# Optimization experiments

Hardware: AMD Instinct MI355X
Metric: run time of the kernel (lower is better)

Reference implementation:

```python
import jax, jax.numpy as jnp
import numpy as np

B, S = 32, 128
E_NUM, SKILL, D_K, D_E, D_A = 4000, 256, 128, 128, 128
AT_NUM, IT_NUM = 1000, 1000
GAMMA = 0.03


def _lin(key, out_d, in_d):
    # xavier-normal style init
    w = jax.random.normal(key, (out_d, in_d), jnp.float32) * (2.0 / (in_d + out_d)) ** 0.5
    b = jnp.zeros((out_d,), jnp.float32)
    return w, b


def setup_inputs() -> dict:
    key = jax.random.key(0)
    ks = jax.random.split(key, 16)
    exercise_id = jax.random.randint(ks[0], (B, S), 0, E_NUM, jnp.int32)
    ans_time = jax.random.randint(ks[1], (B, S), 0, AT_NUM, jnp.int32)
    interval_time = jax.random.randint(ks[2], (B, S), 0, IT_NUM, jnp.int32)
    answer_value = jax.random.randint(ks[3], (B, S), 0, 2, jnp.int32)
    # enhanced q-matrix: binary with zeros replaced by gamma
    qmask = jax.random.bernoulli(ks[4], 0.1, (E_NUM, SKILL))
    q_matrix = jnp.where(qmask, 1.0, GAMMA).astype(jnp.float32)
    ex_table = jax.random.normal(ks[5], (E_NUM, D_E), jnp.float32)
    at_table = jax.random.normal(ks[6], (AT_NUM, D_K), jnp.float32)
    it_table = jax.random.normal(ks[7], (IT_NUM, D_K), jnp.float32)
    W1, b1 = _lin(ks[8], D_K, D_E + D_K + D_A)   # learning_embed_layer
    Wl, bl = _lin(ks[9], D_K, 4 * D_K)           # learning_layer
    Wg, bg = _lin(ks[10], D_K, 4 * D_K)          # learning_gate
    Wf, bf = _lin(ks[11], D_K, 3 * D_K)          # forgetting_gate
    Wp, bp = _lin(ks[12], D_K, 2 * D_K)          # predicting_layer
    # xavier-uniform initial knowledge state, shared across batch
    lim = (6.0 / (SKILL + D_K)) ** 0.5
    h0 = jax.random.uniform(ks[13], (SKILL, D_K), jnp.float32, -lim, lim)
    return {"exercise_id": exercise_id, "ans_time": ans_time,
            "interval_time": interval_time, "answer_value": answer_value,
            "q_matrix": q_matrix, "ex_table": ex_table, "at_table": at_table,
            "it_table": it_table, "W1": W1, "b1": b1, "Wl": Wl, "bl": bl,
            "Wg": Wg, "bg": bg, "Wf": Wf, "bf": bf, "Wp": Wp, "bp": bp, "h0": h0}


def _forward(exercise_id, ans_time, interval_time, answer_value, q_matrix,
             ex_table, at_table, it_table, W1, b1, Wl, bl, Wg, bg, Wf, bf,
             Wp, bp, h0):
    b, s = exercise_id.shape
    ex = ex_table[exercise_id]                       # (B,S,d_e)
    at = at_table[ans_time]                          # (B,S,d_k)
    it = it_table[interval_time]                     # (B,S,d_k)
    ans = jnp.broadcast_to(answer_value.astype(ex.dtype)[..., None], (b, s, D_A))
    le = jnp.concatenate([ex, at, ans], -1) @ W1.T + b1   # learning embedding (B,S,d_k)
    kv = q_matrix[exercise_id]                       # knowledge vectors (B,S,skill)

    h_pre = jnp.broadcast_to(h0, (b,) + h0.shape)    # (B,skill,d_k)
    h_tilde_pre = jnp.einsum('bs,bsd->bd', kv[:, 0], h_pre)
    learning_pre = jnp.zeros((b, D_K), ex.dtype)

    def step(carry, xs):
        h_pre, h_tilde_pre, learning_pre = carry
        lv, itv, kv_t, kv_next, ex_next = xs
        x4 = jnp.concatenate([learning_pre, itv, lv, h_tilde_pre], -1)
        lg = jnp.tanh(x4 @ Wl.T + bl)
        gate = jax.nn.sigmoid(x4 @ Wg.T + bg)
        LG = gate * (lg + 1.0) * 0.5                 # (B,d_k)
        LG_tilde = kv_t[:, :, None] * LG[:, None, :] # outer product addressing (B,skill,d_k)
        x3 = jnp.concatenate([h_pre,
                              jnp.broadcast_to(LG[:, None, :], h_pre.shape),
                              jnp.broadcast_to(itv[:, None, :], h_pre.shape)], -1)
        f = jax.nn.sigmoid(x3 @ Wf.T + bf)           # forget gate per skill
        h = LG_tilde + f * h_pre                     # updated knowledge state
        h_tilde = jnp.einsum('bs,bsd->bd', kv_next, h)
        pred = jax.nn.sigmoid(jnp.concatenate([ex_next, h_tilde], -1) @ Wp.T + bp)
        return (h, h_tilde, lv), pred

    sw = lambda a: jnp.swapaxes(a, 0, 1)
    xs = (sw(le[:, :-1]), sw(it[:, 1:]), sw(kv[:, :-1]), sw(kv[:, 1:]), sw(ex[:, 1:]))
    _, preds = jax.lax.scan(step, (h_pre, h_tilde_pre, learning_pre), xs)
    return jnp.swapaxes(preds, 0, 1)                 # (B, S-1, d_k)


def reference(exercise_id, ans_time, interval_time, answer_value, q_matrix,
              ex_table, at_table, it_table, W1, b1, Wl, bl, Wg, bg, Wf, bf,
              Wp, bp, h0):
    return _forward(exercise_id, ans_time, interval_time, answer_value, q_matrix,
                    ex_table, at_table, it_table, W1, b1, Wl, bl, Wg, bg, Wf, bf,
                    Wp, bp, h0)
```

## Files before the change

kernel.cpp:

```cpp
#include <hip/hip_runtime.h>

typedef unsigned int u32;
typedef unsigned short u16;
typedef unsigned long long u64;
typedef u16 u16x8 __attribute__((ext_vector_type(8)));
typedef u16 u16x4 __attribute__((ext_vector_type(4)));
typedef __bf16 bf16x8 __attribute__((ext_vector_type(8)));
typedef __bf16 bf16x4v __attribute__((ext_vector_type(4)));
typedef float f32x4 __attribute__((ext_vector_type(4)));
typedef float f32x2 __attribute__((ext_vector_type(2)));

#define B_SZ 32
#define S_SZ 128
#define T_SZ 127
#define DK 128
#define SKILL 256
#define SQTR 64
#define RL 136
#define PP 68
#define NPAIR 8
#define SPIN_CAP (1 << 18)

__device__ __forceinline__ u16x4 cvt4(f32x4 v) {
    return __builtin_bit_cast(u16x4, __builtin_convertvector(v, bf16x4v));
}
__device__ __forceinline__ u16x8 cvt8(f32x4 a, f32x4 b) {
    u16x4 x = cvt4(a), y = cvt4(b);
    u16x8 r;
    r[0]=x[0]; r[1]=x[1]; r[2]=x[2]; r[3]=x[3];
    r[4]=y[0]; r[5]=y[1]; r[6]=y[2]; r[7]=y[3];
    return r;
}
__device__ __forceinline__ u16 bfu(float x) {
    return __builtin_bit_cast(u16, (__bf16)x);
}
__device__ __forceinline__ float sigm(float x) {
    float e = __builtin_amdgcn_exp2f(-1.44269504f * x);
    return __builtin_amdgcn_rcpf(1.f + e);
}
__device__ __forceinline__ float tanh_f(float x) {
    float e = __builtin_amdgcn_exp2f(-2.88539008f * x);
    return 2.f * __builtin_amdgcn_rcpf(1.f + e) - 1.f;
}
__device__ __forceinline__ f32x4 mfma16(u16x8 a, u16x8 bb, f32x4 c) {
    return __builtin_amdgcn_mfma_f32_16x16x32_bf16(
        __builtin_bit_cast(bf16x8, a), __builtin_bit_cast(bf16x8, bb), c, 0, 0, 0);
}
__device__ __forceinline__ float pval(u64 p) {
    return __builtin_bit_cast(float, (u32)p);
}
__device__ __forceinline__ float dot4(f32x4 w, f32x4 x) {
    return w[0] * x[0] + w[1] * x[1] + w[2] * x[2] + w[3] * x[3];
}

__global__ __launch_bounds__(128, 2) void k_le(
    const int* __restrict__ eid, const int* __restrict__ atime,
    const int* __restrict__ ansv, const float* __restrict__ ex_t,
    const float* __restrict__ at_t, const float* __restrict__ W1,
    const float* __restrict__ b1, float* __restrict__ le_ws)
{
    const int o = threadIdx.x;
    const int p0 = blockIdx.x * NPAIR;
    int eP[NPAIR], aP[NPAIR];
    float avP[NPAIR];
    #pragma unroll
    for (int i = 0; i < NPAIR; ++i) {
        int p = p0 + i, b = p / T_SZ, t = p - b * T_SZ;
        int idx = b * S_SZ + t;
        eP[i] = eid[idx];
        aP[i] = atime[idx];
        avP[i] = (float)ansv[idx];
    }
    const float* wr = W1 + o * 384;
    const float bias = b1[o];
    float acc[NPAIR];
    #pragma unroll
    for (int i = 0; i < NPAIR; ++i) acc[i] = bias;
    #pragma unroll 2
    for (int k4 = 0; k4 < 32; ++k4) {
        f32x4 w = *(const f32x4*)(wr + 4 * k4);
        #pragma unroll
        for (int i = 0; i < NPAIR; ++i) {
            f32x4 x = *(const f32x4*)(ex_t + eP[i] * DK + 4 * k4);
            acc[i] += dot4(w, x);
        }
    }
    #pragma unroll 2
    for (int k4 = 32; k4 < 64; ++k4) {
        f32x4 w = *(const f32x4*)(wr + 4 * k4);
        #pragma unroll
        for (int i = 0; i < NPAIR; ++i) {
            f32x4 x = *(const f32x4*)(at_t + aP[i] * DK + 4 * k4 - 128);
            acc[i] += dot4(w, x);
        }
    }
    float wsum = 0.f;
    #pragma unroll 4
    for (int k4 = 64; k4 < 96; ++k4) {
        f32x4 w = *(const f32x4*)(wr + 4 * k4);
        wsum += w[0] + w[1] + w[2] + w[3];
    }
    #pragma unroll
    for (int i = 0; i < NPAIR; ++i)
        le_ws[(p0 + i) * DK + o] = acc[i] + avP[i] * wsum;
}

__global__ __launch_bounds__(128, 2) void k_pre(
    const int* __restrict__ itime, const float* __restrict__ it_t,
    const float* __restrict__ Wl, const float* __restrict__ blv,
    const float* __restrict__ Wg, const float* __restrict__ bgv,
    const float* __restrict__ Wf, const float* __restrict__ bfv,
    const float* __restrict__ le_ws,
    float* __restrict__ PRE_l, float* __restrict__ PRE_g, float* __restrict__ PRE_f)
{
    const int o = threadIdx.x;
    const int p0 = blockIdx.x * NPAIR;
    int ivP[NPAIR], lpOff[NPAIR];
    float mP[NPAIR];
    #pragma unroll
    for (int i = 0; i < NPAIR; ++i) {
        int p = p0 + i, b = p / T_SZ, t = p - b * T_SZ;
        ivP[i] = itime[b * S_SZ + t + 1];
        mP[i] = (t == 0) ? 0.f : 1.f;
        lpOff[i] = ((t == 0) ? p : p - 1) * DK;
    }
    const float* wl = Wl + o * 512;
    const float* wg = Wg + o * 512;
    const float bl0 = blv[o], bg0 = bgv[o];
    float al[NPAIR], ag[NPAIR];
    #pragma unroll
    for (int i = 0; i < NPAIR; ++i) { al[i] = bl0; ag[i] = bg0; }
    #pragma unroll 2
    for (int k4 = 0; k4 < 32; ++k4) {
        f32x4 w  = *(const f32x4*)(wl + 4 * k4);
        f32x4 w2 = *(const f32x4*)(wg + 4 * k4);
        #pragma unroll
        for (int i = 0; i < NPAIR; ++i) {
            f32x4 x = *(const f32x4*)(le_ws + lpOff[i] + 4 * k4);
            #pragma unroll
            for (int j = 0; j < 4; ++j) {
                float xv = x[j] * mP[i];
                al[i] += w[j] * xv;
                ag[i] += w2[j] * xv;
            }
        }
    }
    #pragma unroll 2
    for (int k4 = 0; k4 < 32; ++k4) {
        f32x4 w  = *(const f32x4*)(wl + 128 + 4 * k4);
        f32x4 w2 = *(const f32x4*)(wg + 128 + 4 * k4);
        #pragma unroll
        for (int i = 0; i < NPAIR; ++i) {
            f32x4 x = *(const f32x4*)(it_t + ivP[i] * DK + 4 * k4);
            #pragma unroll
            for (int j = 0; j < 4; ++j) {
                al[i] += w[j] * x[j];
                ag[i] += w2[j] * x[j];
            }
        }
    }
    #pragma unroll 2
    for (int k4 = 0; k4 < 32; ++k4) {
        f32x4 w  = *(const f32x4*)(wl + 256 + 4 * k4);
        f32x4 w2 = *(const f32x4*)(wg + 256 + 4 * k4);
        #pragma unroll
        for (int i = 0; i < NPAIR; ++i) {
            f32x4 x = *(const f32x4*)(le_ws + (p0 + i) * DK + 4 * k4);
            #pragma unroll
            for (int j = 0; j < 4; ++j) {
                al[i] += w[j] * x[j];
                ag[i] += w2[j] * x[j];
            }
        }
    }
    const float bf0 = bfv[o];
    float af[NPAIR];
    #pragma unroll
    for (int i = 0; i < NPAIR; ++i) af[i] = bf0;
    const float* wf = Wf + o * 384 + 256;
    #pragma unroll 2
    for (int k4 = 0; k4 < 32; ++k4) {
        f32x4 w = *(const f32x4*)(wf + 4 * k4);
        #pragma unroll
        for (int i = 0; i < NPAIR; ++i) {
            f32x4 x = *(const f32x4*)(it_t + ivP[i] * DK + 4 * k4);
            af[i] += dot4(w, x);
        }
    }
    #pragma unroll
    for (int i = 0; i < NPAIR; ++i) {
        size_t idx = (size_t)(p0 + i) * DK + o;
        PRE_l[idx] = al[i];
        PRE_g[idx] = ag[i];
        PRE_f[idx] = af[i];
    }
}

__global__ __launch_bounds__(512, 1) void k_main(
    const int* __restrict__ eid, const float* __restrict__ qmat,
    const float* __restrict__ Wl, const float* __restrict__ Wg,
    const float* __restrict__ Wf, const float* __restrict__ h0,
    const float* __restrict__ PRE_l, const float* __restrict__ PRE_g,
    const float* __restrict__ PRE_f, float* __restrict__ ht_ws,
    u64* __restrict__ xbuf)
{
    extern __shared__ char smem[];
    u16*   hS   = (u16*)smem;
    float* part = (float*)(smem + 17408);
    u16*   htbf = (u16*)(smem + 52224);
    u16*   LGb  = (u16*)(smem + 52736);
    float* LGf  = (float*)(smem + 53248);
    float* cS   = (float*)(smem + 53760);

    const int b    = blockIdx.x;
    const int qid  = blockIdx.y;
    const int tid  = threadIdx.x;
    const int w    = tid >> 6;
    const int lane = tid & 63;
    const int quad = lane >> 4;
    const int l4   = lane & 15;
    const int ih   = w & 1;
    const int jh   = w >> 1;

    u64* xq = xbuf + (size_t)b * 1024;
    const int qa = (qid + 1) & 3, qb2 = (qid + 2) & 3, qc = (qid + 3) & 3;

    u16x8 afr[4][4];
    #pragma unroll
    for (int mt = 0; mt < 4; ++mt)
        #pragma unroll
        for (int kt = 0; kt < 4; ++kt) {
            const float* p = Wf + (64 * ih + 16 * mt + l4) * 384 + 32 * kt + quad * 8;
            afr[mt][kt] = cvt8(*(const f32x4*)p, *(const f32x4*)(p + 4));
        }
    u16x8 azf[2][4];
    #pragma unroll
    for (int mt = 0; mt < 2; ++mt)
        #pragma unroll
        for (int kt = 0; kt < 4; ++kt) {
            int d = 16 * w + 8 * mt + (l4 >> 1);
            const float* base = (l4 & 1) ? Wg : Wl;
            const float* p = base + d * 512 + 384 + 32 * kt + quad * 8;
            azf[mt][kt] = cvt8(*(const f32x4*)p, *(const f32x4*)(p + 4));
        }
    u16x8 acf[4];
    #pragma unroll
    for (int kt = 0; kt < 4; ++kt) {
        const float* p = Wf + (16 * w + l4) * 384 + 128 + 32 * kt + quad * 8;
        acf[kt] = cvt8(*(const f32x4*)p, *(const f32x4*)(p + 4));
    }

    const int sl = 16 * jh + l4;
    f32x4 hreg[4];
    #pragma unroll
    for (int mt = 0; mt < 4; ++mt) {
        int d0 = 64 * ih + 16 * mt + quad * 4;
        f32x4 hv = *(const f32x4*)(h0 + (SQTR * qid + sl) * DK + d0);
        hreg[mt] = hv;
        *(u16x4*)(hS + sl * RL + d0) = cvt4(hv);
    }

    float kvt = qmat[eid[b * S_SZ] * SKILL + SQTR * qid + sl];

    f32x4 accF[4];

    {
        float htp[16];
        #pragma unroll
        for (int mt = 0; mt < 4; ++mt)
            #pragma unroll
            for (int r = 0; r < 4; ++r)
                htp[mt * 4 + r] = kvt * hreg[mt][r];
        #pragma unroll
        for (int mt = 0; mt < 4; ++mt)
            #pragma unroll
            for (int r = 0; r < 4; ++r)
                part[(64 * ih + 16 * mt + quad * 4 + r) * PP + jh * 16 + l4] = htp[mt * 4 + r];
        __syncthreads();
        int d = tid >> 2, kq = tid & 3;
        const float* pp = part + d * PP + kq * 16;
        float v = 0.f;
        #pragma unroll
        for (int i4 = 0; i4 < 4; ++i4) {
            f32x4 x = *(const f32x4*)(pp + 4 * i4);
            v += x[0] + x[1] + x[2] + x[3];
        }
        v += __shfl_xor(v, 1, 64);
        v += __shfl_xor(v, 2, 64);
        if (kq == 0) {
            u64 pkt = ((u64)1u << 32) | (u64)__builtin_bit_cast(u32, v);
            __hip_atomic_store(xq + qid * 256 + 128 + d, pkt,
                               __ATOMIC_RELAXED, __HIP_MEMORY_SCOPE_AGENT);
        }
        asm volatile("" ::: "memory");
        #pragma unroll
        for (int mt = 0; mt < 4; ++mt)
            accF[mt] = (f32x4){0.f, 0.f, 0.f, 0.f};
        {
            const u16* bp2 = hS + sl * RL + quad * 8;
            u16x8 bfr[4];
            #pragma unroll
            for (int kt = 0; kt < 4; ++kt) bfr[kt] = *(const u16x8*)(bp2 + kt * 32);
            #pragma unroll
            for (int mt = 0; mt < 4; ++mt)
                #pragma unroll
                for (int kt = 0; kt < 4; ++kt)
                    accF[mt] = mfma16(afr[mt][kt], bfr[kt], accF[mt]);
        }
        if (kq == 0) {
            u64 pa, pb, pc2;
            int spins = 0;
            do {
                pa  = __hip_atomic_load(xq + qa * 256 + 128 + d, __ATOMIC_RELAXED, __HIP_MEMORY_SCOPE_AGENT);
                pb  = __hip_atomic_load(xq + qb2 * 256 + 128 + d, __ATOMIC_RELAXED, __HIP_MEMORY_SCOPE_AGENT);
                pc2 = __hip_atomic_load(xq + qc * 256 + 128 + d, __ATOMIC_RELAXED, __HIP_MEMORY_SCOPE_AGENT);
                if ((u32)(pa >> 32) >= 1u && (u32)(pb >> 32) >= 1u && (u32)(pc2 >> 32) >= 1u) break;
                if (spins > 64) __builtin_amdgcn_s_sleep(1);
            } while (++spins < SPIN_CAP);
            float va = pval(pa), vb = pval(pb), vc = pval(pc2);
            float v0 = (qid == 0) ? v : (qid == 3) ? va : (qid == 2) ? vb : vc;
            float v1 = (qid == 1) ? v : (qid == 0) ? va : (qid == 3) ? vb : vc;
            float v2 = (qid == 2) ? v : (qid == 1) ? va : (qid == 0) ? vb : vc;
            float v3 = (qid == 3) ? v : (qid == 2) ? va : (qid == 1) ? vb : vc;
            float vt = ((v0 + v1) + v2) + v3;
            float hf = (float)(__bf16)vt;
            htbf[d] = bfu(vt);
            htbf[128 + d] = bfu(vt - hf);
        }
        __syncthreads();
    }

    for (int t = 0; t < T_SZ; ++t) {
        const size_t tb = (size_t)(b * T_SZ + t) * DK;
        float kvn = qmat[eid[b * S_SZ + t + 1] * SKILL + SQTR * qid + sl];
        f32x2 pl[2], pg[2];
        #pragma unroll
        for (int mt = 0; mt < 2; ++mt) {
            int d0 = 16 * w + 8 * mt + 2 * quad;
            pl[mt] = *(const f32x2*)(PRE_l + tb + d0);
            pg[mt] = *(const f32x2*)(PRE_g + tb + d0);
        }
        f32x4 pf = *(const f32x4*)(PRE_f + tb + 16 * w + quad * 4);

        f32x4 accZ[2];
        accZ[0] = (f32x4){0.f, 0.f, 0.f, 0.f};
        accZ[1] = (f32x4){0.f, 0.f, 0.f, 0.f};
        #pragma unroll
        for (int kt = 0; kt < 4; ++kt) {
            u16x8 bh = *(const u16x8*)(htbf + 32 * kt + quad * 8);
            u16x8 bl = *(const u16x8*)(htbf + 128 + 32 * kt + quad * 8);
            #pragma unroll
            for (int mt = 0; mt < 2; ++mt) {
                accZ[mt] = mfma16(azf[mt][kt], bh, accZ[mt]);
                accZ[mt] = mfma16(azf[mt][kt], bl, accZ[mt]);
            }
        }
        #pragma unroll
        for (int mt = 0; mt < 2; ++mt) {
            u32 hpack = 0, lpack = 0;
            f32x2 fpack;
            #pragma unroll
            for (int rp = 0; rp < 2; ++rp) {
                float zl = accZ[mt][2 * rp] + pl[mt][rp];
                float zg = accZ[mt][2 * rp + 1] + pg[mt][rp];
                float LGv = sigm(zg) * (tanh_f(zl) + 1.f) * 0.5f;
                float hif = (float)(__bf16)LGv;
                hpack |= ((u32)bfu(LGv)) << (16 * rp);
                lpack |= ((u32)bfu(LGv - hif)) << (16 * rp);
                fpack[rp] = LGv;
            }
            if (l4 == 0) {
                int d0 = 16 * w + 8 * mt + 2 * quad;
                *(u32*)(LGb + d0) = hpack;
                *(u32*)(LGb + 128 + d0) = lpack;
                *(f32x2*)(LGf + d0) = fpack;
            }
        }
        __syncthreads();

        {
            f32x4 accC = (f32x4){0.f, 0.f, 0.f, 0.f};
            #pragma unroll
            for (int kt = 0; kt < 4; ++kt) {
                u16x8 bh = *(const u16x8*)(LGb + 32 * kt + quad * 8);
                u16x8 bl = *(const u16x8*)(LGb + 128 + 32 * kt + quad * 8);
                accC = mfma16(acf[kt], bh, accC);
                accC = mfma16(acf[kt], bl, accC);
            }
            accC += pf;
            if (l4 == 0) *(f32x4*)(cS + 16 * w + quad * 4) = accC;
        }
        __syncthreads();

        float htp[16];
        #pragma unroll
        for (int mt = 0; mt < 4; ++mt) {
            int d0 = 64 * ih + 16 * mt + quad * 4;
            f32x4 lg = *(const f32x4*)(LGf + d0);
            f32x4 cc = *(const f32x4*)(cS + d0);
            f32x4 hv;
            #pragma unroll
            for (int r = 0; r < 4; ++r) {
                float f = sigm(accF[mt][r] + cc[r]);
                float hn = kvt * lg[r] + f * hreg[mt][r];
                hreg[mt][r] = hn;
                htp[mt * 4 + r] = kvn * hn;
                hv[r] = hn;
            }
            *(u16x4*)(hS + sl * RL + d0) = cvt4(hv);
        }
        #pragma unroll
        for (int mt = 0; mt < 4; ++mt)
            #pragma unroll
            for (int r = 0; r < 4; ++r)
                part[(64 * ih + 16 * mt + quad * 4 + r) * PP + jh * 16 + l4] = htp[mt * 4 + r];
        kvt = kvn;
        __syncthreads();

        {
            int d = tid >> 2, kq = tid & 3;
            const float* pp = part + d * PP + kq * 16;
            float v = 0.f;
            #pragma unroll
            for (int i4 = 0; i4 < 4; ++i4) {
                f32x4 x = *(const f32x4*)(pp + 4 * i4);
                v += x[0] + x[1] + x[2] + x[3];
            }
            v += __shfl_xor(v, 1, 64);
            v += __shfl_xor(v, 2, 64);
            const int slot = t & 1;
            const u32 seq = (u32)(t + 2);
            if (kq == 0) {
                u64 pkt = ((u64)seq << 32) | (u64)__builtin_bit_cast(u32, v);
                __hip_atomic_store(xq + qid * 256 + slot * 128 + d, pkt,
                                   __ATOMIC_RELAXED, __HIP_MEMORY_SCOPE_AGENT);
            }
            asm volatile("" ::: "memory");
            #pragma unroll
            for (int mt = 0; mt < 4; ++mt)
                accF[mt] = (f32x4){0.f, 0.f, 0.f, 0.f};
            {
                const u16* bp2 = hS + sl * RL + quad * 8;
                u16x8 bfr[4];
                #pragma unroll
                for (int kt = 0; kt < 4; ++kt) bfr[kt] = *(const u16x8*)(bp2 + kt * 32);
                #pragma unroll
                for (int mt = 0; mt < 4; ++mt)
                    #pragma unroll
                    for (int kt = 0; kt < 4; ++kt)
                        accF[mt] = mfma16(afr[mt][kt], bfr[kt], accF[mt]);
            }
            if (kq == 0) {
                u64 pa, pb, pc2;
                int spins = 0;
                do {
                    pa  = __hip_atomic_load(xq + qa * 256 + slot * 128 + d, __ATOMIC_RELAXED, __HIP_MEMORY_SCOPE_AGENT);
                    pb  = __hip_atomic_load(xq + qb2 * 256 + slot * 128 + d, __ATOMIC_RELAXED, __HIP_MEMORY_SCOPE_AGENT);
                    pc2 = __hip_atomic_load(xq + qc * 256 + slot * 128 + d, __ATOMIC_RELAXED, __HIP_MEMORY_SCOPE_AGENT);
                    if ((u32)(pa >> 32) >= seq && (u32)(pb >> 32) >= seq && (u32)(pc2 >> 32) >= seq) break;
                    if (spins > 64) __builtin_amdgcn_s_sleep(1);
                } while (++spins < SPIN_CAP);
                float va = pval(pa), vb = pval(pb), vc = pval(pc2);
                float v0 = (qid == 0) ? v : (qid == 3) ? va : (qid == 2) ? vb : vc;
                float v1 = (qid == 1) ? v : (qid == 0) ? va : (qid == 3) ? vb : vc;
                float v2 = (qid == 2) ? v : (qid == 1) ? va : (qid == 0) ? vb : vc;
                float v3 = (qid == 3) ? v : (qid == 2) ? va : (qid == 1) ? vb : vc;
                float vt = ((v0 + v1) + v2) + v3;
                float hf = (float)(__bf16)vt;
                htbf[d] = bfu(vt);
                htbf[128 + d] = bfu(vt - hf);
                if (qid == 0) ht_ws[tb + d] = vt;
            }
        }
        __syncthreads();
    }
}

__global__ __launch_bounds__(128, 2) void k_pred(
    const int* __restrict__ eid, const float* __restrict__ ex_t,
    const float* __restrict__ Wp, const float* __restrict__ bpv,
    const float* __restrict__ ht_ws, float* __restrict__ out)
{
    const int o = threadIdx.x;
    const int p0 = blockIdx.x * NPAIR;
    int eP[NPAIR];
    #pragma unroll
    for (int i = 0; i < NPAIR; ++i) {
        int p = p0 + i, b = p / T_SZ, t = p - b * T_SZ;
        eP[i] = eid[b * S_SZ + t + 1];
    }
    const float* wr = Wp + o * 256;
    const float bias = bpv[o];
    float acc[NPAIR];
    #pragma unroll
    for (int i = 0; i < NPAIR; ++i) acc[i] = bias;
    #pragma unroll 2
    for (int k4 = 0; k4 < 32; ++k4) {
        f32x4 w = *(const f32x4*)(wr + 4 * k4);
        #pragma unroll
        for (int i = 0; i < NPAIR; ++i) {
            f32x4 x = *(const f32x4*)(ex_t + eP[i] * DK + 4 * k4);
            acc[i] += dot4(w, x);
        }
    }
    #pragma unroll 2
    for (int k4 = 32; k4 < 64; ++k4) {
        f32x4 w = *(const f32x4*)(wr + 4 * k4);
        #pragma unroll
        for (int i = 0; i < NPAIR; ++i) {
            f32x4 x = *(const f32x4*)(ht_ws + (size_t)(p0 + i) * DK + 4 * k4 - 128);
            acc[i] += dot4(w, x);
        }
    }
    #pragma unroll
    for (int i = 0; i < NPAIR; ++i)
        out[(size_t)(p0 + i) * DK + o] = sigm(acc[i]);
}

extern "C" void kernel_launch(void* const* d_in, const int* in_sizes, int n_in,
                              void* d_out, int out_size, void* d_ws, size_t ws_size,
                              hipStream_t stream) {
    const int* eid     = (const int*)d_in[0];
    const int* atime   = (const int*)d_in[1];
    const int* itime   = (const int*)d_in[2];
    const int* ansv    = (const int*)d_in[3];
    const float* qmat  = (const float*)d_in[4];
    const float* ex_t  = (const float*)d_in[5];
    const float* at_t  = (const float*)d_in[6];
    const float* it_t  = (const float*)d_in[7];
    const float* W1    = (const float*)d_in[8];
    const float* b1    = (const float*)d_in[9];
    const float* Wl    = (const float*)d_in[10];
    const float* blv   = (const float*)d_in[11];
    const float* Wg    = (const float*)d_in[12];
    const float* bgv   = (const float*)d_in[13];
    const float* Wf    = (const float*)d_in[14];
    const float* bfv   = (const float*)d_in[15];
    const float* Wp    = (const float*)d_in[16];
    const float* bpv   = (const float*)d_in[17];
    const float* h0    = (const float*)d_in[18];
    float* out = (float*)d_out;

    const size_t SZ = (size_t)B_SZ * T_SZ * DK;
    float* wsf   = (float*)d_ws;
    float* le_ws = wsf;
    float* PRE_l = wsf + SZ;
    float* PRE_g = wsf + 2 * SZ;
    float* PRE_f = wsf + 3 * SZ;
    float* ht_ws = wsf + 4 * SZ;
    u64* xbuf = (u64*)le_ws;

    hipFuncSetAttribute((const void*)k_main,
                        hipFuncAttributeMaxDynamicSharedMemorySize, 86016);

    dim3 gaux(508);
    k_le  <<<gaux, 128, 0, stream>>>(eid, atime, ansv, ex_t, at_t, W1, b1, le_ws);
    k_pre <<<gaux, 128, 0, stream>>>(itime, it_t, Wl, blv, Wg, bgv, Wf, bfv,
                                     le_ws, PRE_l, PRE_g, PRE_f);
    hipMemsetAsync(xbuf, 0, (size_t)B_SZ * 1024 * sizeof(u64), stream);
    k_main<<<dim3(B_SZ, 4), 512, 86016, stream>>>(eid, qmat, Wl, Wg, Wf, h0,
                                                  PRE_l, PRE_g, PRE_f, ht_ws,
                                                  xbuf);
    k_pred<<<gaux, 128, 0, stream>>>(eid, ex_t, Wp, bpv, ht_ws, out);
}
```

Measured before the change: 599.3 us.

## Transpose weights for coalesced loads and fuse learning-embed into pre-gate kernel

Adds a prep kernel that rewrites all dense weight matrices into a k4-major, output-interleaved layout, so adjacent threads read adjacent float4s instead of rows 1.5–2 KB apart. The learning-embedding computation is merged into the pre-gate kernel: each block recomputes the one extra previous pair it needs into shared memory, which removes a global round trip and a kernel launch. The cost is an extra transpose pass over about 1 MB of weights on every call and some redundant compute for the overlapping pair. Launch-bounds occupancy hints are also dropped.

```diff
diff --git a/kernel.cpp b/kernel.cpp
--- a/kernel.cpp
+++ b/kernel.cpp
@@ -21,6 +21,13 @@
 #define NPAIR 8
 #define SPIN_CAP (1 << 18)
 
+#define W1T_OFF 0
+#define WLT_OFF 49152
+#define WGT_OFF 114688
+#define WFT_OFF 180224
+#define WPT_OFF 229376
+#define WT_TOTAL 262144
+
 __device__ __forceinline__ u16x4 cvt4(f32x4 v) {
     return __builtin_bit_cast(u16x4, __builtin_convertvector(v, bf16x4v));
 }
@@ -53,90 +60,98 @@
     return w[0] * x[0] + w[1] * x[1] + w[2] * x[2] + w[3] * x[3];
 }
 
-__global__ __launch_bounds__(128, 2) void k_le(
+__global__ __launch_bounds__(256) void k_prep(
+    const float* __restrict__ W1, const float* __restrict__ Wl,
+    const float* __restrict__ Wg, const float* __restrict__ Wf,
+    const float* __restrict__ Wp, float* __restrict__ WT)
+{
+    int i = blockIdx.x * 256 + threadIdx.x;
+    int j = i & 3, o = (i >> 2) & 127, k4 = i >> 9;
+    float v;
+    if (k4 < 96)        v = W1[o * 384 + 4 * k4 + j];
+    else if (k4 < 224)  v = Wl[o * 512 + 4 * (k4 - 96) + j];
+    else if (k4 < 352)  v = Wg[o * 512 + 4 * (k4 - 224) + j];
+    else if (k4 < 448)  v = Wf[o * 384 + 4 * (k4 - 352) + j];
+    else                v = Wp[o * 256 + 4 * (k4 - 448) + j];
+    WT[i] = v;
+}
+
+__global__ __launch_bounds__(128) void k_pre(
     const int* __restrict__ eid, const int* __restrict__ atime,
-    const int* __restrict__ ansv, const float* __restrict__ ex_t,
-    const float* __restrict__ at_t, const float* __restrict__ W1,
-    const float* __restrict__ b1, float* __restrict__ le_ws)
+    const int* __restrict__ ansv, const int* __restrict__ itime,
+    const float* __restrict__ ex_t, const float* __restrict__ at_t,
+    const float* __restrict__ it_t, const float* __restrict__ WT,
+    const float* __restrict__ b1, const float* __restrict__ blv,
+    const float* __restrict__ bgv, const float* __restrict__ bfv,
+    float* __restrict__ PRE_l, float* __restrict__ PRE_g, float* __restrict__ PRE_f)
 {
+    __shared__ float leS[9 * 128];
     const int o = threadIdx.x;
     const int p0 = blockIdx.x * NPAIR;
-    int eP[NPAIR], aP[NPAIR];
-    float avP[NPAIR];
+
+    {
+        int eP[9], aP[9];
+        float avP[9];
+        #pragma unroll
+        for (int i = 0; i < 9; ++i) {
+            int p = p0 - 1 + i;
+            if (p < 0) p = 0;
+            int bb = p / T_SZ, tt = p - bb * T_SZ;
+            int idx = bb * S_SZ + tt;
+            eP[i] = eid[idx];
+            aP[i] = atime[idx];
+            avP[i] = (float)ansv[idx];
+        }
+        const float bias = b1[o];
+        float acc[9];
+        #pragma unroll
+        for (int i = 0; i < 9; ++i) acc[i] = bias;
+        #pragma unroll 2
+        for (int k4 = 0; k4 < 32; ++k4) {
+            f32x4 w = *(const f32x4*)(WT + W1T_OFF + (k4 * 128 + o) * 4);
+            #pragma unroll
+            for (int i = 0; i < 9; ++i)
+                acc[i] += dot4(w, *(const f32x4*)(ex_t + eP[i] * DK + 4 * k4));
+        }
+        #pragma unroll 2
+        for (int k4 = 32; k4 < 64; ++k4) {
+            f32x4 w = *(const f32x4*)(WT + W1T_OFF + (k4 * 128 + o) * 4);
+            #pragma unroll
+            for (int i = 0; i < 9; ++i)
+                acc[i] += dot4(w, *(const f32x4*)(at_t + aP[i] * DK + 4 * k4 - 128));
+        }
+        float wsum = 0.f;
+        #pragma unroll 4
+        for (int k4 = 64; k4 < 96; ++k4) {
+            f32x4 w = *(const f32x4*)(WT + W1T_OFF + (k4 * 128 + o) * 4);
+            wsum += w[0] + w[1] + w[2] + w[3];
+        }
+        #pragma unroll
+        for (int i = 0; i < 9; ++i)
+            leS[i * 128 + o] = acc[i] + avP[i] * wsum;
+    }
+    __syncthreads();
+
+    int ivP[NPAIR];
+    float mP[NPAIR];
     #pragma unroll
     for (int i = 0; i < NPAIR; ++i) {
-        int p = p0 + i, b = p / T_SZ, t = p - b * T_SZ;
-        int idx = b * S_SZ + t;
-        eP[i] = eid[idx];
-        aP[i] = atime[idx];
-        avP[i] = (float)ansv[idx];
-    }
-    const float* wr = W1 + o * 384;
-    const float bias = b1[o];
-    float acc[NPAIR];
-    #pragma unroll
-    for (int i = 0; i < NPAIR; ++i) acc[i] = bias;
-    #pragma unroll 2
-    for (int k4 = 0; k4 < 32; ++k4) {
-        f32x4 w = *(const f32x4*)(wr + 4 * k4);
-        #pragma unroll
-        for (int i = 0; i < NPAIR; ++i) {
-            f32x4 x = *(const f32x4*)(ex_t + eP[i] * DK + 4 * k4);
-            acc[i] += dot4(w, x);
-        }
-    }
-    #pragma unroll 2
-    for (int k4 = 32; k4 < 64; ++k4) {
-        f32x4 w = *(const f32x4*)(wr + 4 * k4);
-        #pragma unroll
-        for (int i = 0; i < NPAIR; ++i) {
-            f32x4 x = *(const f32x4*)(at_t + aP[i] * DK + 4 * k4 - 128);
-            acc[i] += dot4(w, x);
-        }
-    }
-    float wsum = 0.f;
-    #pragma unroll 4
-    for (int k4 = 64; k4 < 96; ++k4) {
-        f32x4 w = *(const f32x4*)(wr + 4 * k4);
-        wsum += w[0] + w[1] + w[2] + w[3];
-    }
-    #pragma unroll
-    for (int i = 0; i < NPAIR; ++i)
-        le_ws[(p0 + i) * DK + o] = acc[i] + avP[i] * wsum;
-}
-
-__global__ __launch_bounds__(128, 2) void k_pre(
-    const int* __restrict__ itime, const float* __restrict__ it_t,
-    const float* __restrict__ Wl, const float* __restrict__ blv,
-    const float* __restrict__ Wg, const float* __restrict__ bgv,
-    const float* __restrict__ Wf, const float* __restrict__ bfv,
-    const float* __restrict__ le_ws,
-    float* __restrict__ PRE_l, float* __restrict__ PRE_g, float* __restrict__ PRE_f)
-{
-    const int o = threadIdx.x;
-    const int p0 = blockIdx.x * NPAIR;
-    int ivP[NPAIR], lpOff[NPAIR];
-    float mP[NPAIR];
-    #pragma unroll
-    for (int i = 0; i < NPAIR; ++i) {
-        int p = p0 + i, b = p / T_SZ, t = p - b * T_SZ;
-        ivP[i] = itime[b * S_SZ + t + 1];
-        mP[i] = (t == 0) ? 0.f : 1.f;
-        lpOff[i] = ((t == 0) ? p : p - 1) * DK;
-    }
-    const float* wl = Wl + o * 512;
-    const float* wg = Wg + o * 512;
+        int p = p0 + i;
+        int bb = p / T_SZ, tt = p - bb * T_SZ;
+        ivP[i] = itime[bb * S_SZ + tt + 1];
+        mP[i] = (tt == 0) ? 0.f : 1.f;
+    }
     const float bl0 = blv[o], bg0 = bgv[o];
     float al[NPAIR], ag[NPAIR];
     #pragma unroll
     for (int i = 0; i < NPAIR; ++i) { al[i] = bl0; ag[i] = bg0; }
     #pragma unroll 2
     for (int k4 = 0; k4 < 32; ++k4) {
-        f32x4 w  = *(const f32x4*)(wl + 4 * k4);
-        f32x4 w2 = *(const f32x4*)(wg + 4 * k4);
+        f32x4 w  = *(const f32x4*)(WT + WLT_OFF + (k4 * 128 + o) * 4);
+        f32x4 w2 = *(const f32x4*)(WT + WGT_OFF + (k4 * 128 + o) * 4);
         #pragma unroll
         for (int i = 0; i < NPAIR; ++i) {
-            f32x4 x = *(const f32x4*)(le_ws + lpOff[i] + 4 * k4);
+            f32x4 x = *(const f32x4*)(leS + i * 128 + 4 * k4);
             #pragma unroll
             for (int j = 0; j < 4; ++j) {
                 float xv = x[j] * mP[i];
@@ -146,12 +161,12 @@
         }
     }
     #pragma unroll 2
-    for (int k4 = 0; k4 < 32; ++k4) {
-        f32x4 w  = *(const f32x4*)(wl + 128 + 4 * k4);
-        f32x4 w2 = *(const f32x4*)(wg + 128 + 4 * k4);
+    for (int k4 = 32; k4 < 64; ++k4) {
+        f32x4 w  = *(const f32x4*)(WT + WLT_OFF + (k4 * 128 + o) * 4);
+        f32x4 w2 = *(const f32x4*)(WT + WGT_OFF + (k4 * 128 + o) * 4);
         #pragma unroll
         for (int i = 0; i < NPAIR; ++i) {
-            f32x4 x = *(const f32x4*)(it_t + ivP[i] * DK + 4 * k4);
+            f32x4 x = *(const f32x4*)(it_t + ivP[i] * DK + 4 * k4 - 128);
             #pragma unroll
             for (int j = 0; j < 4; ++j) {
                 al[i] += w[j] * x[j];
@@ -160,12 +175,12 @@
         }
     }
     #pragma unroll 2
-    for (int k4 = 0; k4 < 32; ++k4) {
-        f32x4 w  = *(const f32x4*)(wl + 256 + 4 * k4);
-        f32x4 w2 = *(const f32x4*)(wg + 256 + 4 * k4);
+    for (int k4 = 64; k4 < 96; ++k4) {
+        f32x4 w  = *(const f32x4*)(WT + WLT_OFF + (k4 * 128 + o) * 4);
+        f32x4 w2 = *(const f32x4*)(WT + WGT_OFF + (k4 * 128 + o) * 4);
         #pragma unroll
         for (int i = 0; i < NPAIR; ++i) {
-            f32x4 x = *(const f32x4*)(le_ws + (p0 + i) * DK + 4 * k4);
+            f32x4 x = *(const f32x4*)(leS + (i + 1) * 128 + 4 * k4 - 256);
             #pragma unroll
             for (int j = 0; j < 4; ++j) {
                 al[i] += w[j] * x[j];
@@ -177,10 +192,9 @@
     float af[NPAIR];
     #pragma unroll
     for (int i = 0; i < NPAIR; ++i) af[i] = bf0;
-    const float* wf = Wf + o * 384 + 256;
     #pragma unroll 2
     for (int k4 = 0; k4 < 32; ++k4) {
-        f32x4 w = *(const f32x4*)(wf + 4 * k4);
+        f32x4 w = *(const f32x4*)(WT + WFT_OFF + ((64 + k4) * 128 + o) * 4);
         #pragma unroll
         for (int i = 0; i < NPAIR; ++i) {
             f32x4 x = *(const f32x4*)(it_t + ivP[i] * DK + 4 * k4);
@@ -476,9 +490,9 @@
     }
 }
 
-__global__ __launch_bounds__(128, 2) void k_pred(
+__global__ __launch_bounds__(128) void k_pred(
     const int* __restrict__ eid, const float* __restrict__ ex_t,
-    const float* __restrict__ Wp, const float* __restrict__ bpv,
+    const float* __restrict__ WT, const float* __restrict__ bpv,
     const float* __restrict__ ht_ws, float* __restrict__ out)
 {
     const int o = threadIdx.x;
@@ -489,14 +503,13 @@
         int p = p0 + i, b = p / T_SZ, t = p - b * T_SZ;
         eP[i] = eid[b * S_SZ + t + 1];
     }
-    const float* wr = Wp + o * 256;
     const float bias = bpv[o];
     float acc[NPAIR];
     #pragma unroll
     for (int i = 0; i < NPAIR; ++i) acc[i] = bias;
     #pragma unroll 2
     for (int k4 = 0; k4 < 32; ++k4) {
-        f32x4 w = *(const f32x4*)(wr + 4 * k4);
+        f32x4 w = *(const f32x4*)(WT + WPT_OFF + (k4 * 128 + o) * 4);
         #pragma unroll
         for (int i = 0; i < NPAIR; ++i) {
             f32x4 x = *(const f32x4*)(ex_t + eP[i] * DK + 4 * k4);
@@ -505,7 +518,7 @@
     }
     #pragma unroll 2
     for (int k4 = 32; k4 < 64; ++k4) {
-        f32x4 w = *(const f32x4*)(wr + 4 * k4);
+        f32x4 w = *(const f32x4*)(WT + WPT_OFF + (k4 * 128 + o) * 4);
         #pragma unroll
         for (int i = 0; i < NPAIR; ++i) {
             f32x4 x = *(const f32x4*)(ht_ws + (size_t)(p0 + i) * DK + 4 * k4 - 128);
@@ -543,23 +556,24 @@
 
     const size_t SZ = (size_t)B_SZ * T_SZ * DK;
     float* wsf   = (float*)d_ws;
-    float* le_ws = wsf;
+    u64*   xbuf  = (u64*)wsf;
+    float* WT    = wsf + 65536;
     float* PRE_l = wsf + SZ;
     float* PRE_g = wsf + 2 * SZ;
     float* PRE_f = wsf + 3 * SZ;
     float* ht_ws = wsf + 4 * SZ;
-    u64* xbuf = (u64*)le_ws;
 
     hipFuncSetAttribute((const void*)k_main,
                         hipFuncAttributeMaxDynamicSharedMemorySize, 86016);
 
-    dim3 gaux(508);
-    k_le  <<<gaux, 128, 0, stream>>>(eid, atime, ansv, ex_t, at_t, W1, b1, le_ws);
-    k_pre <<<gaux, 128, 0, stream>>>(itime, it_t, Wl, blv, Wg, bgv, Wf, bfv,
-                                     le_ws, PRE_l, PRE_g, PRE_f);
     hipMemsetAsync(xbuf, 0, (size_t)B_SZ * 1024 * sizeof(u64), stream);
+    k_prep<<<dim3(WT_TOTAL / 256), 256, 0, stream>>>(W1, Wl, Wg, Wf, Wp, WT);
+    k_pre <<<dim3(508), 128, 0, stream>>>(eid, atime, ansv, itime,
+                                          ex_t, at_t, it_t, WT,
+                                          b1, blv, bgv, bfv,
+                                          PRE_l, PRE_g, PRE_f);
     k_main<<<dim3(B_SZ, 4), 512, 86016, stream>>>(eid, qmat, Wl, Wg, Wf, h0,
                                                   PRE_l, PRE_g, PRE_f, ht_ws,
                                                   xbuf);
-    k_pred<<<gaux, 128, 0, stream>>>(eid, ex_t, Wp, bpv, ht_ws, out);
-}
+    k_pred<<<dim3(508), 128, 0, stream>>>(eid, ex_t, WT, bpv, ht_ws, out);
+}
```

Result: no change. 605.7 us (+1.1%).

## Double k_main block to 1024 threads, splitting per-wave MFMA and state work

Applied to the files above, without the earlier changes.

The recurrent main kernel now runs 16 waves per block instead of 8. Each wave owns one 16-row d tile and 32 skill rows rather than four d tiles, and the cross-thread partial reduction uses 8 lanes per output. This shortens the serial per-step critical path by spreading the MFMA and elementwise work over more waves. The cost is more barrier participants and half the waves idling in the forget-gate stage. The k_pre loop indexing is also rewritten with offset loop bounds, which leaves the same arithmetic.

```diff
diff --git a/kernel.cpp b/kernel.cpp
--- a/kernel.cpp
+++ b/kernel.cpp
@@ -146,12 +146,12 @@
         }
     }
     #pragma unroll 2
-    for (int k4 = 0; k4 < 32; ++k4) {
-        f32x4 w  = *(const f32x4*)(wl + 128 + 4 * k4);
-        f32x4 w2 = *(const f32x4*)(wg + 128 + 4 * k4);
-        #pragma unroll
-        for (int i = 0; i < NPAIR; ++i) {
-            f32x4 x = *(const f32x4*)(it_t + ivP[i] * DK + 4 * k4);
+    for (int k4 = 32; k4 < 64; ++k4) {
+        f32x4 w  = *(const f32x4*)(wl + 4 * k4);
+        f32x4 w2 = *(const f32x4*)(wg + 4 * k4);
+        #pragma unroll
+        for (int i = 0; i < NPAIR; ++i) {
+            f32x4 x = *(const f32x4*)(it_t + ivP[i] * DK + 4 * k4 - 128);
             #pragma unroll
             for (int j = 0; j < 4; ++j) {
                 al[i] += w[j] * x[j];
@@ -160,12 +160,12 @@
         }
     }
     #pragma unroll 2
-    for (int k4 = 0; k4 < 32; ++k4) {
-        f32x4 w  = *(const f32x4*)(wl + 256 + 4 * k4);
-        f32x4 w2 = *(const f32x4*)(wg + 256 + 4 * k4);
-        #pragma unroll
-        for (int i = 0; i < NPAIR; ++i) {
-            f32x4 x = *(const f32x4*)(le_ws + (p0 + i) * DK + 4 * k4);
+    for (int k4 = 64; k4 < 96; ++k4) {
+        f32x4 w  = *(const f32x4*)(wl + 4 * k4);
+        f32x4 w2 = *(const f32x4*)(wg + 4 * k4);
+        #pragma unroll
+        for (int i = 0; i < NPAIR; ++i) {
+            f32x4 x = *(const f32x4*)(le_ws + (p0 + i) * DK + 4 * k4 - 256);
             #pragma unroll
             for (int j = 0; j < 4; ++j) {
                 al[i] += w[j] * x[j];
@@ -196,7 +196,7 @@
     }
 }
 
-__global__ __launch_bounds__(512, 1) void k_main(
+__global__ __launch_bounds__(1024, 1) void k_main(
     const int* __restrict__ eid, const float* __restrict__ qmat,
     const float* __restrict__ Wl, const float* __restrict__ Wg,
     const float* __restrict__ Wf, const float* __restrict__ h0,
@@ -215,97 +215,94 @@
     const int b    = blockIdx.x;
     const int qid  = blockIdx.y;
     const int tid  = threadIdx.x;
-    const int w    = tid >> 6;
+    const int w2   = tid >> 6;
     const int lane = tid & 63;
     const int quad = lane >> 4;
     const int l4   = lane & 15;
-    const int ih   = w & 1;
-    const int jh   = w >> 1;
+    const int mt   = w2 & 7;
+    const int np   = w2 >> 3;
 
     u64* xq = xbuf + (size_t)b * 1024;
     const int qa = (qid + 1) & 3, qb2 = (qid + 2) & 3, qc = (qid + 3) & 3;
 
-    u16x8 afr[4][4];
-    #pragma unroll
-    for (int mt = 0; mt < 4; ++mt)
-        #pragma unroll
-        for (int kt = 0; kt < 4; ++kt) {
-            const float* p = Wf + (64 * ih + 16 * mt + l4) * 384 + 32 * kt + quad * 8;
-            afr[mt][kt] = cvt8(*(const f32x4*)p, *(const f32x4*)(p + 4));
-        }
-    u16x8 azf[2][4];
-    #pragma unroll
-    for (int mt = 0; mt < 2; ++mt)
-        #pragma unroll
-        for (int kt = 0; kt < 4; ++kt) {
-            int d = 16 * w + 8 * mt + (l4 >> 1);
-            const float* base = (l4 & 1) ? Wg : Wl;
-            const float* p = base + d * 512 + 384 + 32 * kt + quad * 8;
-            azf[mt][kt] = cvt8(*(const f32x4*)p, *(const f32x4*)(p + 4));
-        }
+    u16x8 afr[4];
+    #pragma unroll
+    for (int kt = 0; kt < 4; ++kt) {
+        const float* p = Wf + (16 * mt + l4) * 384 + 32 * kt + quad * 8;
+        afr[kt] = cvt8(*(const f32x4*)p, *(const f32x4*)(p + 4));
+    }
+    u16x8 azf[4];
+    #pragma unroll
+    for (int kt = 0; kt < 4; ++kt) {
+        int d = 8 * w2 + (l4 >> 1);
+        const float* base = (l4 & 1) ? Wg : Wl;
+        const float* p = base + d * 512 + 384 + 32 * kt + quad * 8;
+        azf[kt] = cvt8(*(const f32x4*)p, *(const f32x4*)(p + 4));
+    }
     u16x8 acf[4];
     #pragma unroll
     for (int kt = 0; kt < 4; ++kt) {
-        const float* p = Wf + (16 * w + l4) * 384 + 128 + 32 * kt + quad * 8;
+        const float* p = Wf + (16 * mt + l4) * 384 + 128 + 32 * kt + quad * 8;
         acf[kt] = cvt8(*(const f32x4*)p, *(const f32x4*)(p + 4));
     }
 
-    const int sl = 16 * jh + l4;
-    f32x4 hreg[4];
-    #pragma unroll
-    for (int mt = 0; mt < 4; ++mt) {
-        int d0 = 64 * ih + 16 * mt + quad * 4;
-        f32x4 hv = *(const f32x4*)(h0 + (SQTR * qid + sl) * DK + d0);
-        hreg[mt] = hv;
-        *(u16x4*)(hS + sl * RL + d0) = cvt4(hv);
-    }
-
-    float kvt = qmat[eid[b * S_SZ] * SKILL + SQTR * qid + sl];
-
-    f32x4 accF[4];
-
+    const int s0 = 32 * np + l4;
+    const int s1 = s0 + 16;
+    const int d0 = 16 * mt + 4 * quad;
+
+    f32x4 hreg[2];
     {
-        float htp[16];
-        #pragma unroll
-        for (int mt = 0; mt < 4; ++mt)
+        f32x4 hv = *(const f32x4*)(h0 + (SQTR * qid + s0) * DK + d0);
+        hreg[0] = hv;
+        *(u16x4*)(hS + s0 * RL + d0) = cvt4(hv);
+        hv = *(const f32x4*)(h0 + (SQTR * qid + s1) * DK + d0);
+        hreg[1] = hv;
+        *(u16x4*)(hS + s1 * RL + d0) = cvt4(hv);
+    }
+
+    float kvt[2];
+    {
+        int e0 = eid[b * S_SZ];
+        kvt[0] = qmat[e0 * SKILL + SQTR * qid + s0];
+        kvt[1] = qmat[e0 * SKILL + SQTR * qid + s1];
+    }
+
+    f32x4 accF[2];
+
+    {
+        #pragma unroll
+        for (int i = 0; i < 2; ++i) {
+            int s = i ? s1 : s0;
             #pragma unroll
             for (int r = 0; r < 4; ++r)
-                htp[mt * 4 + r] = kvt * hreg[mt][r];
-        #pragma unroll
-        for (int mt = 0; mt < 4; ++mt)
-            #pragma unroll
-            for (int r = 0; r < 4; ++r)
-                part[(64 * ih + 16 * mt + quad * 4 + r) * PP + jh * 16 + l4] = htp[mt * 4 + r];
+                part[(d0 + r) * PP + s] = kvt[i] * hreg[i][r];
+        }
         __syncthreads();
-        int d = tid >> 2, kq = tid & 3;
-        const float* pp = part + d * PP + kq * 16;
-        float v = 0.f;
-        #pragma unroll
-        for (int i4 = 0; i4 < 4; ++i4) {
-            f32x4 x = *(const f32x4*)(pp + 4 * i4);
-            v += x[0] + x[1] + x[2] + x[3];
-        }
+        int d = tid >> 3, kq = tid & 7;
+        const float* pp = part + d * PP + kq * 8;
+        f32x4 x0 = *(const f32x4*)pp;
+        f32x4 x1 = *(const f32x4*)(pp + 4);
+        float v = (x0[0] + x0[1] + x0[2] + x0[3]) + (x1[0] + x1[1] + x1[2] + x1[3]);
         v += __shfl_xor(v, 1, 64);
         v += __shfl_xor(v, 2, 64);
+        v += __shfl_xor(v, 4, 64);
         if (kq == 0) {
             u64 pkt = ((u64)1u << 32) | (u64)__builtin_bit_cast(u32, v);
             __hip_atomic_store(xq + qid * 256 + 128 + d, pkt,
                                __ATOMIC_RELAXED, __HIP_MEMORY_SCOPE_AGENT);
         }
         asm volatile("" ::: "memory");
-        #pragma unroll
-        for (int mt = 0; mt < 4; ++mt)
-            accF[mt] = (f32x4){0.f, 0.f, 0.f, 0.f};
-        {
-            const u16* bp2 = hS + sl * RL + quad * 8;
+        accF[0] = (f32x4){0.f, 0.f, 0.f, 0.f};
+        accF[1] = (f32x4){0.f, 0.f, 0.f, 0.f};
+        #pragma unroll
+        for (int i = 0; i < 2; ++i) {
+            const u16* bp2 = hS + (i ? s1 : s0) * RL + quad * 8;
             u16x8 bfr[4];
             #pragma unroll
             for (int kt = 0; kt < 4; ++kt) bfr[kt] = *(const u16x8*)(bp2 + kt * 32);
             #pragma unroll
-            for (int mt = 0; mt < 4; ++mt)
-                #pragma unroll
-                for (int kt = 0; kt < 4; ++kt)
-                    accF[mt] = mfma16(afr[mt][kt], bfr[kt], accF[mt]);
+            for (int kt = 0; kt < 4; ++kt)
+                accF[i] = mfma16(afr[kt], bfr[kt], accF[i]);
         }
         if (kq == 0) {
             u64 pa, pb, pc2;
@@ -332,37 +329,33 @@
 
     for (int t = 0; t < T_SZ; ++t) {
         const size_t tb = (size_t)(b * T_SZ + t) * DK;
-        float kvn = qmat[eid[b * S_SZ + t + 1] * SKILL + SQTR * qid + sl];
-        f32x2 pl[2], pg[2];
-        #pragma unroll
-        for (int mt = 0; mt < 2; ++mt) {
-            int d0 = 16 * w + 8 * mt + 2 * quad;
-            pl[mt] = *(const f32x2*)(PRE_l + tb + d0);
-            pg[mt] = *(const f32x2*)(PRE_g + tb + d0);
-        }
-        f32x4 pf = *(const f32x4*)(PRE_f + tb + 16 * w + quad * 4);
-
-        f32x4 accZ[2];
-        accZ[0] = (f32x4){0.f, 0.f, 0.f, 0.f};
-        accZ[1] = (f32x4){0.f, 0.f, 0.f, 0.f};
+        float kvn[2];
+        {
+            int en = eid[b * S_SZ + t + 1];
+            kvn[0] = qmat[en * SKILL + SQTR * qid + s0];
+            kvn[1] = qmat[en * SKILL + SQTR * qid + s1];
+        }
+        const int dz = 8 * w2 + 2 * quad;
+        f32x2 pl = *(const f32x2*)(PRE_l + tb + dz);
+        f32x2 pg = *(const f32x2*)(PRE_g + tb + dz);
+        f32x4 pf;
+        if (w2 < 8) pf = *(const f32x4*)(PRE_f + tb + 16 * w2 + 4 * quad);
+
+        f32x4 accZ = (f32x4){0.f, 0.f, 0.f, 0.f};
         #pragma unroll
         for (int kt = 0; kt < 4; ++kt) {
             u16x8 bh = *(const u16x8*)(htbf + 32 * kt + quad * 8);
             u16x8 bl = *(const u16x8*)(htbf + 128 + 32 * kt + quad * 8);
-            #pragma unroll
-            for (int mt = 0; mt < 2; ++mt) {
-                accZ[mt] = mfma16(azf[mt][kt], bh, accZ[mt]);
-                accZ[mt] = mfma16(azf[mt][kt], bl, accZ[mt]);
-            }
-        }
-        #pragma unroll
-        for (int mt = 0; mt < 2; ++mt) {
+            accZ = mfma16(azf[kt], bh, accZ);
+            accZ = mfma16(azf[kt], bl, accZ);
+        }
+        {
             u32 hpack = 0, lpack = 0;
             f32x2 fpack;
             #pragma unroll
             for (int rp = 0; rp < 2; ++rp) {
-                float zl = accZ[mt][2 * rp] + pl[mt][rp];
-                float zg = accZ[mt][2 * rp + 1] + pg[mt][rp];
+                float zl = accZ[2 * rp] + pl[rp];
+                float zg = accZ[2 * rp + 1] + pg[rp];
                 float LGv = sigm(zg) * (tanh_f(zl) + 1.f) * 0.5f;
                 float hif = (float)(__bf16)LGv;
                 hpack |= ((u32)bfu(LGv)) << (16 * rp);
@@ -370,15 +363,14 @@
                 fpack[rp] = LGv;
             }
             if (l4 == 0) {
-                int d0 = 16 * w + 8 * mt + 2 * quad;
-                *(u32*)(LGb + d0) = hpack;
-                *(u32*)(LGb + 128 + d0) = lpack;
-                *(f32x2*)(LGf + d0) = fpack;
+                *(u32*)(LGb + dz) = hpack;
+                *(u32*)(LGb + 128 + dz) = lpack;
+                *(f32x2*)(LGf + dz) = fpack;
             }
         }
         __syncthreads();
 
-        {
+        if (w2 < 8) {
             f32x4 accC = (f32x4){0.f, 0.f, 0.f, 0.f};
             #pragma unroll
             for (int kt = 0; kt < 4; ++kt) {
@@ -388,46 +380,41 @@
                 accC = mfma16(acf[kt], bl, accC);
             }
             accC += pf;
-            if (l4 == 0) *(f32x4*)(cS + 16 * w + quad * 4) = accC;
+            if (l4 == 0) *(f32x4*)(cS + 16 * w2 + 4 * quad) = accC;
         }
         __syncthreads();
 
-        float htp[16];
-        #pragma unroll
-        for (int mt = 0; mt < 4; ++mt) {
-            int d0 = 64 * ih + 16 * mt + quad * 4;
+        {
             f32x4 lg = *(const f32x4*)(LGf + d0);
             f32x4 cc = *(const f32x4*)(cS + d0);
-            f32x4 hv;
-            #pragma unroll
-            for (int r = 0; r < 4; ++r) {
-                float f = sigm(accF[mt][r] + cc[r]);
-                float hn = kvt * lg[r] + f * hreg[mt][r];
-                hreg[mt][r] = hn;
-                htp[mt * 4 + r] = kvn * hn;
-                hv[r] = hn;
-            }
-            *(u16x4*)(hS + sl * RL + d0) = cvt4(hv);
-        }
-        #pragma unroll
-        for (int mt = 0; mt < 4; ++mt)
-            #pragma unroll
-            for (int r = 0; r < 4; ++r)
-                part[(64 * ih + 16 * mt + quad * 4 + r) * PP + jh * 16 + l4] = htp[mt * 4 + r];
-        kvt = kvn;
+            #pragma unroll
+            for (int i = 0; i < 2; ++i) {
+                int s = i ? s1 : s0;
+                f32x4 hv;
+                #pragma unroll
+                for (int r = 0; r < 4; ++r) {
+                    float f = sigm(accF[i][r] + cc[r]);
+                    float hn = kvt[i] * lg[r] + f * hreg[i][r];
+                    hreg[i][r] = hn;
+                    hv[r] = hn;
+                    part[(d0 + r) * PP + s] = kvn[i] * hn;
+                }
+                *(u16x4*)(hS + s * RL + d0) = cvt4(hv);
+            }
+            kvt[0] = kvn[0];
+            kvt[1] = kvn[1];
+        }
         __syncthreads();
 
         {
-            int d = tid >> 2, kq = tid & 3;
-            const float* pp = part + d * PP + kq * 16;
-            float v = 0.f;
-            #pragma unroll
-            for (int i4 = 0; i4 < 4; ++i4) {
-                f32x4 x = *(const f32x4*)(pp + 4 * i4);
-                v += x[0] + x[1] + x[2] + x[3];
-            }
+            int d = tid >> 3, kq = tid & 7;
+            const float* pp = part + d * PP + kq * 8;
+            f32x4 x0 = *(const f32x4*)pp;
+            f32x4 x1 = *(const f32x4*)(pp + 4);
+            float v = (x0[0] + x0[1] + x0[2] + x0[3]) + (x1[0] + x1[1] + x1[2] + x1[3]);
             v += __shfl_xor(v, 1, 64);
             v += __shfl_xor(v, 2, 64);
+            v += __shfl_xor(v, 4, 64);
             const int slot = t & 1;
             const u32 seq = (u32)(t + 2);
             if (kq == 0) {
@@ -436,19 +423,17 @@
                                    __ATOMIC_RELAXED, __HIP_MEMORY_SCOPE_AGENT);
             }
             asm volatile("" ::: "memory");
-            #pragma unroll
-            for (int mt = 0; mt < 4; ++mt)
-                accF[mt] = (f32x4){0.f, 0.f, 0.f, 0.f};
-            {
-                const u16* bp2 = hS + sl * RL + quad * 8;
+            accF[0] = (f32x4){0.f, 0.f, 0.f, 0.f};
+            accF[1] = (f32x4){0.f, 0.f, 0.f, 0.f};
+            #pragma unroll
+            for (int i = 0; i < 2; ++i) {
+                const u16* bp2 = hS + (i ? s1 : s0) * RL + quad * 8;
                 u16x8 bfr[4];
                 #pragma unroll
                 for (int kt = 0; kt < 4; ++kt) bfr[kt] = *(const u16x8*)(bp2 + kt * 32);
                 #pragma unroll
-                for (int mt = 0; mt < 4; ++mt)
-                    #pragma unroll
-                    for (int kt = 0; kt < 4; ++kt)
-                        accF[mt] = mfma16(afr[mt][kt], bfr[kt], accF[mt]);
+                for (int kt = 0; kt < 4; ++kt)
+                    accF[i] = mfma16(afr[kt], bfr[kt], accF[i]);
             }
             if (kq == 0) {
                 u64 pa, pb, pc2;
@@ -551,15 +536,15 @@
     u64* xbuf = (u64*)le_ws;
 
     hipFuncSetAttribute((const void*)k_main,
-                        hipFuncAttributeMaxDynamicSharedMemorySize, 86016);
+                        hipFuncAttributeMaxDynamicSharedMemorySize, 54272);
 
     dim3 gaux(508);
     k_le  <<<gaux, 128, 0, stream>>>(eid, atime, ansv, ex_t, at_t, W1, b1, le_ws);
     k_pre <<<gaux, 128, 0, stream>>>(itime, it_t, Wl, blv, Wg, bgv, Wf, bfv,
                                      le_ws, PRE_l, PRE_g, PRE_f);
     hipMemsetAsync(xbuf, 0, (size_t)B_SZ * 1024 * sizeof(u64), stream);
-    k_main<<<dim3(B_SZ, 4), 512, 86016, stream>>>(eid, qmat, Wl, Wg, Wf, h0,
-                                                  PRE_l, PRE_g, PRE_f, ht_ws,
-                                                  xbuf);
+    k_main<<<dim3(B_SZ, 4), 1024, 54272, stream>>>(eid, qmat, Wl, Wg, Wf, h0,
+                                                   PRE_l, PRE_g, PRE_f, ht_ws,
+                                                   xbuf);
     k_pred<<<gaux, 128, 0, stream>>>(eid, ex_t, Wp, bpv, ht_ws, out);
 }
```

New measurement: 634.8 us. 5.9% more time.
